# Kernel tuning notes

Measured on AMD Instinct MI355X. Metric: run time of the kernel, lower is better.

Reference implementation:

```python
import jax, jax.numpy as jnp
import numpy as np

T = 2048      # total tokens (single prefill sequence)
HID = 2048    # hidden_size
H = 16        # num k-heads == num v-heads
DK = 128      # key head dim
DV = 128      # value head dim
K = 4         # causal conv kernel width
EPS = 1e-6


def setup_inputs() -> dict:
    key = jax.random.key(0)
    ks = jax.random.split(key, 10)
    n = lambda k, shape, sc: (jax.random.normal(k, shape, jnp.float32) * sc)
    return {
        "hidden_states": n(ks[0], (T, HID), 1.0),
        "Wq": n(ks[1], (HID, H * DK), 0.02),
        "Wk": n(ks[2], (HID, H * DK), 0.02),
        "Wv": n(ks[3], (HID, H * DV), 0.02),
        "Wb": n(ks[4], (HID, H), 0.02),
        "conv_wq": n(ks[5], (H * DK, K), 0.5),
        "conv_wk": n(ks[6], (H * DK, K), 0.5),
        "conv_wv": n(ks[7], (H * DV, K), 0.5),
        "o_norm_w": jnp.ones((DV,), jnp.float32),
        "Wo": n(ks[8], (HID, HID), 0.02),
    }


def _causal_conv_silu(x, w):
    # x: [T, D], w: [D, K] depthwise causal conv, then SiLU (matches causal_conv1d_fn)
    xp = jnp.pad(x, ((K - 1, 0), (0, 0)))
    y = sum(xp[j:j + T] * w[:, j] for j in range(K))
    return jax.nn.silu(y)


def _l2norm(x):
    return x * jax.lax.rsqrt(jnp.sum(x * x, axis=-1, keepdims=True) + EPS)


def reference(hidden_states, Wq, Wk, Wv, Wb, conv_wq, conv_wk, conv_wv, o_norm_w, Wo):
    # projections [T, H*D]
    q = _causal_conv_silu(hidden_states @ Wq, conv_wq).reshape(T, H, DK)
    k = _causal_conv_silu(hidden_states @ Wk, conv_wk).reshape(T, H, DK)
    v = _causal_conv_silu(hidden_states @ Wv, conv_wv).reshape(T, H, DV)
    beta = jax.nn.sigmoid(hidden_states @ Wb)  # [T, H]

    # qk l2-norm + scale (FLA chunk_delta_rule defaults)
    q = _l2norm(q) * (DK ** -0.5)
    k = _l2norm(k)

    # delta-rule recurrence: S <- S + beta * k (v - k^T S)
    def step(S, inp):
        q_t, k_t, v_t, b_t = inp            # [H,DK],[H,DK],[H,DV],[H]
        kS = jnp.einsum('hk,hkv->hv', k_t, S)
        delta = b_t[:, None] * (v_t - kS)   # [H, DV]
        S = S + jnp.einsum('hk,hv->hkv', k_t, delta)
        o_t = jnp.einsum('hk,hkv->hv', q_t, S)
        return S, o_t

    S0 = jnp.zeros((H, DK, DV), jnp.float32)
    _, o = jax.lax.scan(step, S0, (q, k, v, beta))  # o: [T, H, DV]

    # per-head RMSNorm on value head dim
    o = o * jax.lax.rsqrt(jnp.mean(o * o, axis=-1, keepdims=True) + EPS) * o_norm_w
    out = o.reshape(T, H * DV) @ Wo
    return out
```

## Files before the change

kernel.cpp:

```cpp
#include <hip/hip_runtime.h>

typedef unsigned short u16;
typedef __attribute__((ext_vector_type(4))) unsigned short u16x4;
typedef __attribute__((ext_vector_type(8))) unsigned short u16x8;
typedef __attribute__((ext_vector_type(8))) short short8;
typedef __attribute__((ext_vector_type(4))) float f32x4;

#define DEVI __device__ __forceinline__

DEVI u16 f2b(float f) {
  union { float f; unsigned u; } x; x.f = f;
  unsigned r = (x.u + 0x7fffu + ((x.u >> 16) & 1u)) >> 16;
  return (u16)r;
}
DEVI float b2f(u16 h) {
  union { unsigned u; float f; } x; x.u = ((unsigned)h) << 16;
  return x.f;
}
DEVI f32x4 mfma_bf16(short8 a, short8 b, f32x4 c) {
  return __builtin_amdgcn_mfma_f32_16x16x32_bf16(a, b, c, 0, 0, 0);
}
DEVI void gl2lds16(const u16* g, u16* l) {
  __builtin_amdgcn_global_load_lds((__attribute__((address_space(1))) void*)g,
                                   (__attribute__((address_space(3))) void*)l,
                                   16, 0, 0);
}
DEVI void barrier_lds() {
  asm volatile("s_waitcnt lgkmcnt(0)\n\ts_barrier" ::: "memory");
}

__global__ void k_cvt(const float* __restrict__ src, u16* __restrict__ dst, int n4) {
  int i = blockIdx.x * 256 + threadIdx.x;
  if (i < n4) {
    float4 v = ((const float4*)src)[i];
    u16x4 r; r.x = f2b(v.x); r.y = f2b(v.y); r.z = f2b(v.z); r.w = f2b(v.w);
    ((u16x4*)dst)[i] = r;
  }
}

__global__ void k_transpose(const float* __restrict__ src, u16* __restrict__ dst, int R, int C) {
  __shared__ float tile[32][33];
  int bx = blockIdx.x << 5, by = blockIdx.y << 5;
  int x = threadIdx.x, y = threadIdx.y;
#pragma unroll
  for (int j = 0; j < 32; j += 8)
    tile[y + j][x] = src[(size_t)(by + y + j) * C + bx + x];
  __syncthreads();
#pragma unroll
  for (int j = 0; j < 32; j += 8)
    dst[(size_t)(bx + y + j) * R + by + x] = f2b(tile[x][y + j]);
}

__global__ __launch_bounds__(256, 2)
void k_gemm_bt(const u16* __restrict__ A, const u16* __restrict__ BT,
               float* __restrict__ Cf, u16* __restrict__ Cb,
               int M, int N, int K, int outbf) {
  __shared__ __align__(16) u16 As[4096];
  __shared__ __align__(16) u16 Bs[4096];
  const int tid = threadIdx.x, wave = tid >> 6, lane = tid & 63;
  const long bm = (long)blockIdx.y << 7, bn = (long)blockIdx.x << 7;
  const int r0 = (wave << 4) + (lane >> 2), kof = (lane & 3) << 3;
  const u16* gA = A + (bm + r0) * (long)K + kof;
  const u16* gB = BT + (bn + r0) * (long)K + kof;
  u16* lA = As + (wave << 9);
  u16* lB = Bs + (wave << 9);
  const long stepR = (long)64 * K;
  const int wr = (wave >> 1) << 6, wc = (wave & 1) << 6;
  const int fr = lane & 15, fq = (lane >> 4) << 3;
  f32x4 acc[4][4];
#pragma unroll
  for (int i = 0; i < 4; ++i)
#pragma unroll
    for (int j = 0; j < 4; ++j) acc[i][j] = (f32x4){0.f, 0.f, 0.f, 0.f};
  for (int k0 = 0; k0 < K; k0 += 32) {
    gl2lds16(gA + k0, lA);
    gl2lds16(gA + stepR + k0, lA + 2048);
    gl2lds16(gB + k0, lB);
    gl2lds16(gB + stepR + k0, lB + 2048);
    __syncthreads();
    short8 af[4], bfr[4];
#pragma unroll
    for (int t = 0; t < 4; ++t)
      af[t] = *(const short8*)&As[(wr + (t << 4) + fr) * 32 + fq];
#pragma unroll
    for (int t = 0; t < 4; ++t)
      bfr[t] = *(const short8*)&Bs[(wc + (t << 4) + fr) * 32 + fq];
#pragma unroll
    for (int i = 0; i < 4; ++i)
#pragma unroll
      for (int j = 0; j < 4; ++j)
        acc[i][j] = mfma_bf16(af[i], bfr[j], acc[i][j]);
    __syncthreads();
  }
  const int er = (lane >> 4) << 2, ec = lane & 15;
#pragma unroll
  for (int i = 0; i < 4; ++i)
#pragma unroll
    for (int j = 0; j < 4; ++j)
#pragma unroll
      for (int r = 0; r < 4; ++r) {
        long row = bm + wr + (i << 4) + er + r;
        long col = bn + wc + (j << 4) + ec;
        if (outbf) Cb[row * N + col] = f2b(acc[i][j][r]);
        else       Cf[row * N + col] = acc[i][j][r];
      }
}

__global__ void k_wbT(const float* __restrict__ src, u16* __restrict__ dst) {
  int j = blockIdx.x * 256 + threadIdx.x;
  int n = j >> 11, k = j & 2047;
  dst[j] = f2b(src[k * 16 + n]);
}

__global__ __launch_bounds__(256, 4)
void k_beta(const u16* __restrict__ Xb, const u16* __restrict__ WbT,
            float* __restrict__ beta) {
  __shared__ float part[4][256];
  int tid = threadIdx.x, w = tid >> 6, lane = tid & 63;
  int t0 = blockIdx.x << 4;
  int fr = lane & 15, fq = (lane >> 4) << 3;
  const u16* ap = Xb + (size_t)(t0 + fr) * 2048 + (w << 9) + fq;
  const u16* bp = WbT + (size_t)fr * 2048 + (w << 9) + fq;
  f32x4 acc = {0.f, 0.f, 0.f, 0.f};
#pragma unroll
  for (int ks = 0; ks < 16; ++ks)
    acc = mfma_bf16(*(const short8*)(ap + (ks << 5)), *(const short8*)(bp + (ks << 5)), acc);
  int er = (lane >> 4) << 2;
#pragma unroll
  for (int r = 0; r < 4; ++r) part[w][(er + r) * 16 + fr] = acc[r];
  __syncthreads();
  float s = part[0][tid] + part[1][tid] + part[2][tid] + part[3][tid];
  beta[(t0 << 4) + tid] = 1.f / (1.f + __expf(-s));
}

__global__ void k_conv(const u16* __restrict__ qkv,
                       const float* __restrict__ cwq, const float* __restrict__ cwk,
                       const float* __restrict__ cwv,
                       u16* __restrict__ qn, u16* __restrict__ kn, u16* __restrict__ vn) {
  int t = blockIdx.x, s = blockIdx.y;
  int kind = s >> 4, h = s & 15, d = threadIdx.x;
  int col = kind * 2048 + (h << 7) + d;
  const float* cw = (kind == 0) ? cwq : ((kind == 1) ? cwk : cwv);
  float4 w = *(const float4*)(cw + (size_t)((h << 7) + d) * 4);
  float x[4];
#pragma unroll
  for (int j = 0; j < 4; ++j) {
    int tt = t - 3 + j;
    x[j] = (tt >= 0) ? b2f(qkv[(size_t)tt * 6144 + col]) : 0.f;
  }
  float y = x[0] * w.x + x[1] * w.y + x[2] * w.z + x[3] * w.w;
  y = y / (1.f + __expf(-y));
  float sc = 1.f;
  __shared__ float red[2];
  if (kind < 2) {
    float ss = y * y;
#pragma unroll
    for (int off = 32; off; off >>= 1) ss += __shfl_down(ss, off, 64);
    int lane = threadIdx.x & 63, wv = threadIdx.x >> 6;
    if (lane == 0) red[wv] = ss;
    __syncthreads();
    float tot = red[0] + red[1];
    sc = rsqrtf(tot + 1e-6f);
    if (kind == 0) sc *= 0.08838834764831843f;
  }
  u16* dst = (kind == 0) ? qn : ((kind == 1) ? kn : vn);
  dst[((size_t)h << 18) + ((size_t)t << 7) + d] = f2b(y * sc);
}

__global__ __launch_bounds__(256, 2)
void k_prep(const u16* __restrict__ qn, const u16* __restrict__ kn, const u16* __restrict__ vn,
            const float* __restrict__ beta,
            u16* __restrict__ Gg, u16* __restrict__ Wg,
            u16* __restrict__ KTg, u16* __restrict__ UTg) {
  __shared__ __align__(16) char sm[70912];
  u16*  Kc  = (u16*)sm;
  u16*  Qc  = (u16*)(sm + 17408);
  u16*  Vc  = (u16*)(sm + 34816);
  u16*  KTl = (u16*)(sm + 52224);
  float* AL = (float*)(sm + 52224);
  float* Bl = (float*)(sm + 70656);
  u16*  WR  = Qc;
  int h = blockIdx.x, c = blockIdx.y;
  int tid = threadIdx.x, wave = tid >> 6, lane = tid & 63;
  size_t ch = (size_t)(c * 16 + h);
  const u16* kb = kn + ((size_t)h << 18) + ((size_t)c << 13);
  const u16* qb = qn + ((size_t)h << 18) + ((size_t)c << 13);
  const u16* vb = vn + ((size_t)h << 18) + ((size_t)c << 13);
#pragma unroll
  for (int s = 0; s < 4; ++s) {
    int e = (tid + (s << 8)) << 3;
    int t = e >> 7, d = e & 127;
    *(u16x8*)&Kc[t * 136 + d] = *(const u16x8*)(kb + e);
    *(u16x8*)&Qc[t * 136 + d] = *(const u16x8*)(qb + e);
    *(u16x8*)&Vc[t * 136 + d] = *(const u16x8*)(vb + e);
  }
  if (tid < 64) Bl[tid] = beta[((c << 6) + tid) * 16 + h];
  __syncthreads();
  int fr = lane & 15, fq = (lane >> 4) << 3, q4 = (lane >> 4) << 2;
  int arow = (wave << 4) + fr;
  f32x4 kk[4], qk[4];
#pragma unroll
  for (int ct = 0; ct < 4; ++ct) { kk[ct] = (f32x4){0.f,0.f,0.f,0.f}; qk[ct] = (f32x4){0.f,0.f,0.f,0.f}; }
#pragma unroll
  for (int ks = 0; ks < 4; ++ks) {
    short8 aK = *(const short8*)&Kc[arow * 136 + (ks << 5) + fq];
    short8 aQ = *(const short8*)&Qc[arow * 136 + (ks << 5) + fq];
#pragma unroll
    for (int ct = 0; ct < 4; ++ct) {
      short8 bK = *(const short8*)&Kc[((ct << 4) + fr) * 136 + (ks << 5) + fq];
      kk[ct] = mfma_bf16(aK, bK, kk[ct]);
      qk[ct] = mfma_bf16(aQ, bK, qk[ct]);
    }
  }
#pragma unroll
  for (int ct = 0; ct < 4; ++ct)
#pragma unroll
    for (int r = 0; r < 4; ++r) {
      int i = (wave << 4) + q4 + r, j = (ct << 4) + fr;
      Gg[(ch << 12) + i * 64 + j] = f2b((j <= i) ? qk[ct][r] : 0.f);
    }
  {
    int d = tid & 127, tg = tid >> 7;
#pragma unroll
    for (int it = 0; it < 4; ++it) {
      int t0 = (tg + (it << 1)) << 3;
      u16x8 pk;
#pragma unroll
      for (int j = 0; j < 8; ++j) pk[j] = Kc[(t0 + j) * 136 + d];
      *(u16x8*)&KTl[d * 72 + t0] = pk;
    }
  }
  __syncthreads();
#pragma unroll
  for (int it = 0; it < 4; ++it) {
    int idx = tid + (it << 8);
    int row = idx >> 3, j8 = (idx & 7) << 3;
    *(u16x8*)(KTg + (ch << 13) + (row << 6) + j8) = *(const u16x8*)&KTl[row * 72 + j8];
  }
  __syncthreads();
  {
    float bi[4];
#pragma unroll
    for (int r = 0; r < 4; ++r) bi[r] = Bl[(wave << 4) + q4 + r];
#pragma unroll
    for (int ct = 0; ct < 4; ++ct)
#pragma unroll
      for (int r = 0; r < 4; ++r) {
        int i = (wave << 4) + q4 + r, j = (ct << 4) + fr;
        AL[i * 64 + j] = (j < i) ? bi[r] * kk[ct][r] : 0.f;
      }
  }
  __syncthreads();
  float X[64];
  {
    const u16* colp = (tid < 128) ? (Kc + tid) : (Vc + (tid - 128));
#pragma unroll
    for (int t = 0; t < 64; ++t) X[t] = Bl[t] * b2f(colp[t * 136]);
#pragma unroll
    for (int r = 1; r < 64; ++r) {
      float s = 0.f;
      const float* Ar = &AL[r * 64];
      int r4 = r & ~3;
#pragma unroll
      for (int l = 0; l < 64; l += 4)
        if (l + 4 <= r) {
          float4 a = *(const float4*)(Ar + l);
          s += a.x * X[l] + a.y * X[l + 1] + a.z * X[l + 2] + a.w * X[l + 3];
        }
#pragma unroll
      for (int l = 0; l < 4; ++l)
        if (r4 + l < r) s += Ar[r4 + l] * X[r4 + l];
      X[r] -= s;
    }
  }
  __syncthreads();
  if (tid < 128) {
#pragma unroll
    for (int t = 0; t < 64; ++t) WR[t * 136 + tid] = f2b(X[t]);
  } else {
    int v = tid - 128;
    u16* dstr = UTg + (ch << 13) + (v << 6);
#pragma unroll
    for (int j = 0; j < 8; ++j) {
      u16x8 p;
#pragma unroll
      for (int e = 0; e < 8; ++e) p[e] = f2b(X[(j << 3) + e]);
      *(u16x8*)(dstr + (j << 3)) = p;
    }
  }
  __syncthreads();
#pragma unroll
  for (int it = 0; it < 4; ++it) {
    int idx = tid + (it << 8);
    int row = idx >> 4, j8 = (idx & 15) << 3;
    *(u16x8*)(Wg + (ch << 13) + (row << 7) + j8) = *(const u16x8*)&WR[row * 136 + j8];
  }
}

struct Frags { short8 q[4], w[4], g[2], k[4]; u16x4 u; };

DEVI void load_frags(Frags& f, const u16* qh, const u16* Wg, const u16* Gg,
                     const u16* KTg, const u16* UTg, int c, int h,
                     int trow, int fr, int fq, int q4, int w, int vbase) {
  const u16* qb = qh + ((size_t)((c << 6) + trow + fr) << 7) + fq;
#pragma unroll
  for (int ks = 0; ks < 4; ++ks) f.q[ks] = *(const short8*)(qb + (ks << 5));
  size_t ch = (size_t)(c * 16 + h);
  const u16* wb = Wg + (ch << 13) + ((size_t)(trow + fr) << 7) + fq;
#pragma unroll
  for (int ks = 0; ks < 4; ++ks) f.w[ks] = *(const short8*)(wb + (ks << 5));
  const u16* gb = Gg + (ch << 12) + ((size_t)(trow + fr) << 6) + fq;
#pragma unroll
  for (int ks = 0; ks < 2; ++ks) f.g[ks] = *(const short8*)(gb + (ks << 5));
  const u16* kbp = KTg + (ch << 13) + ((size_t)(w << 5) << 6) + fq;
#pragma unroll
  for (int dt = 0; dt < 2; ++dt)
#pragma unroll
    for (int ks = 0; ks < 2; ++ks)
      f.k[(dt << 1) | ks] = *(const short8*)(kbp + ((size_t)((dt << 4) + fr) << 6) + (ks << 5));
  f.u = *(const u16x4*)(UTg + (ch << 13) + ((size_t)(vbase + fr) << 6) + trow + q4);
}

DEVI void chunk_body(int c, Frags& f, u16* ST, u16* DT, float* oh,
                     int trow, int fr, int fq, int q4, int w, int vbase,
                     f32x4& S0, f32x4& S1) {
#pragma unroll
  for (int r = 0; r < 4; ++r) {
    ST[(q4 + r) * 136 + (w << 5) + fr] = f2b(S0[r]);
    ST[(q4 + r) * 136 + (w << 5) + 16 + fr] = f2b(S1[r]);
  }
  barrier_lds();
  short8 sf[4];
#pragma unroll
  for (int ks = 0; ks < 4; ++ks) sf[ks] = *(const short8*)&ST[fr * 136 + (ks << 5) + fq];
  f32x4 racc = {0.f,0.f,0.f,0.f}, oacc = {0.f,0.f,0.f,0.f};
#pragma unroll
  for (int ks = 0; ks < 4; ++ks) {
    racc = mfma_bf16(f.w[ks], sf[ks], racc);
    oacc = mfma_bf16(f.q[ks], sf[ks], oacc);
  }
#pragma unroll
  for (int r = 0; r < 4; ++r)
    DT[fr * 72 + trow + q4 + r] = f2b(b2f(f.u[r]) - racc[r]);
  barrier_lds();
  short8 df[2];
#pragma unroll
  for (int ks = 0; ks < 2; ++ks) df[ks] = *(const short8*)&DT[fr * 72 + (ks << 5) + fq];
#pragma unroll
  for (int ks = 0; ks < 2; ++ks) {
    oacc = mfma_bf16(f.g[ks], df[ks], oacc);
    S0 = mfma_bf16(df[ks], f.k[ks], S0);
    S1 = mfma_bf16(df[ks], f.k[2 | ks], S1);
  }
#pragma unroll
  for (int r = 0; r < 4; ++r)
    oh[(size_t)((c << 6) + trow + q4 + r) * 128 + vbase + fr] = oacc[r];
}

__global__ __launch_bounds__(256, 1)
void k_delta(const u16* __restrict__ qn, const u16* __restrict__ Wg,
             const u16* __restrict__ Gg, const u16* __restrict__ KTg,
             const u16* __restrict__ UTg, float* __restrict__ o) {
  __shared__ __align__(16) u16 ST[16 * 136];
  __shared__ __align__(16) u16 DT[16 * 72];
  int bx = blockIdx.x;
  int h = bx & 15, vbase = (bx >> 4) << 4;
  int tid = threadIdx.x, w = tid >> 6, lane = tid & 63;
  int fr = lane & 15, fq = (lane >> 4) << 3, q4 = (lane >> 4) << 2;
  int trow = w << 4;
  const u16* qh = qn + ((size_t)h << 18);
  float* oh = o + ((size_t)h << 18);
  f32x4 S0 = {0.f,0.f,0.f,0.f}, S1 = {0.f,0.f,0.f,0.f};
  Frags fa, fb;
  load_frags(fa, qh, Wg, Gg, KTg, UTg, 0, h, trow, fr, fq, q4, w, vbase);
  for (int c = 0; c < 32; c += 2) {
    int c1 = c + 1, c2 = (c + 2 < 32) ? c + 2 : 31;
    load_frags(fb, qh, Wg, Gg, KTg, UTg, c1, h, trow, fr, fq, q4, w, vbase);
    chunk_body(c, fa, ST, DT, oh, trow, fr, fq, q4, w, vbase, S0, S1);
    load_frags(fa, qh, Wg, Gg, KTg, UTg, c2, h, trow, fr, fq, q4, w, vbase);
    chunk_body(c1, fb, ST, DT, oh, trow, fr, fq, q4, w, vbase, S0, S1);
  }
}

__global__ void k_onorm(const float* __restrict__ o, const float* __restrict__ onw,
                        u16* __restrict__ onb) {
  int t = blockIdx.x, h = blockIdx.y, d = threadIdx.x;
  float x = o[((size_t)h << 18) + ((size_t)t << 7) + d];
  float ss = x * x;
#pragma unroll
  for (int off = 32; off; off >>= 1) ss += __shfl_down(ss, off, 64);
  __shared__ float red[2];
  int lane = d & 63, wv = d >> 6;
  if (lane == 0) red[wv] = ss;
  __syncthreads();
  float tot = red[0] + red[1];
  float y = x * rsqrtf(tot * (1.f / 128.f) + 1e-6f) * onw[d];
  onb[((size_t)t << 11) + (h << 7) + d] = f2b(y);
}

extern "C" void kernel_launch(void* const* d_in, const int* in_sizes, int n_in,
                              void* d_out, int out_size, void* d_ws, size_t ws_size,
                              hipStream_t stream) {
  (void)in_sizes; (void)n_in; (void)out_size; (void)ws_size;
  const float* hs  = (const float*)d_in[0];
  const float* Wq  = (const float*)d_in[1];
  const float* Wk  = (const float*)d_in[2];
  const float* Wv  = (const float*)d_in[3];
  const float* Wb  = (const float*)d_in[4];
  const float* cwq = (const float*)d_in[5];
  const float* cwk = (const float*)d_in[6];
  const float* cwv = (const float*)d_in[7];
  const float* onw = (const float*)d_in[8];
  const float* Wo  = (const float*)d_in[9];
  float* out = (float*)d_out;
  char* ws = (char*)d_ws;
  const size_t MB = 1ull << 20;
  u16*  Xb   = (u16*)(ws);
  u16*  WT   = (u16*)(ws + 8  * MB);
  u16*  WoT  = (u16*)(ws + 32 * MB);
  u16*  QKV  = (u16*)(ws + 40 * MB);
  u16*  Wg   = (u16*)(ws + 40 * MB);
  u16*  KTg  = (u16*)(ws + 48 * MB);
  u16*  UTg  = (u16*)(ws + 56 * MB);
  u16*  qn_  = (u16*)(ws + 64 * MB);
  u16*  kn_  = (u16*)(ws + 72 * MB);
  u16*  vn_  = (u16*)(ws + 80 * MB);
  float* beta= (float*)(ws + 88 * MB);
  u16*  WbT  = (u16*)(ws + 88 * MB + 512 * 1024);
  u16*  Gm   = (u16*)(ws + 89 * MB);
  float* o_  = (float*)(ws + 93 * MB);
  u16*  onb  = (u16*)(ws + 109 * MB);

  dim3 tb(32, 8);
  k_cvt<<<4096, 256, 0, stream>>>(hs, Xb, 2048 * 2048 / 4);
  k_wbT<<<128, 256, 0, stream>>>(Wb, WbT);
  k_transpose<<<dim3(64, 64), tb, 0, stream>>>(Wq, WT,                   2048, 2048);
  k_transpose<<<dim3(64, 64), tb, 0, stream>>>(Wk, WT + 2048 * 2048,     2048, 2048);
  k_transpose<<<dim3(64, 64), tb, 0, stream>>>(Wv, WT + 2 * 2048 * 2048, 2048, 2048);
  k_transpose<<<dim3(64, 64), tb, 0, stream>>>(Wo, WoT,                  2048, 2048);
  k_gemm_bt<<<dim3(48, 16), 256, 0, stream>>>(Xb, WT, nullptr, QKV, 2048, 6144, 2048, 1);
  k_beta<<<128, 256, 0, stream>>>(Xb, WbT, beta);
  k_conv<<<dim3(2048, 48), 128, 0, stream>>>(QKV, cwq, cwk, cwv, qn_, kn_, vn_);
  k_prep<<<dim3(16, 32), 256, 0, stream>>>(qn_, kn_, vn_, beta, Gm, Wg, KTg, UTg);
  k_delta<<<128, 256, 0, stream>>>(qn_, Wg, Gm, KTg, UTg, o_);
  k_onorm<<<dim3(2048, 16), 128, 0, stream>>>(o_, onw, onb);
  k_gemm_bt<<<dim3(16, 16), 256, 0, stream>>>(onb, WoT, out, nullptr, 2048, 2048, 2048, 0);
}
```

Baseline: 399.6 us.

## Fuse preprocessing launches, widen transpose tiles, and swizzle GEMM LDS layout

```diff
diff --git a/kernel.cpp b/kernel.cpp
--- a/kernel.cpp
+++ b/kernel.cpp
@@ -29,26 +29,45 @@
   asm volatile("s_waitcnt lgkmcnt(0)\n\ts_barrier" ::: "memory");
 }
 
-__global__ void k_cvt(const float* __restrict__ src, u16* __restrict__ dst, int n4) {
-  int i = blockIdx.x * 256 + threadIdx.x;
-  if (i < n4) {
-    float4 v = ((const float4*)src)[i];
-    u16x4 r; r.x = f2b(v.x); r.y = f2b(v.y); r.z = f2b(v.z); r.w = f2b(v.w);
-    ((u16x4*)dst)[i] = r;
-  }
-}
-
-__global__ void k_transpose(const float* __restrict__ src, u16* __restrict__ dst, int R, int C) {
-  __shared__ float tile[32][33];
-  int bx = blockIdx.x << 5, by = blockIdx.y << 5;
-  int x = threadIdx.x, y = threadIdx.y;
-#pragma unroll
-  for (int j = 0; j < 32; j += 8)
-    tile[y + j][x] = src[(size_t)(by + y + j) * C + bx + x];
-  __syncthreads();
-#pragma unroll
-  for (int j = 0; j < 32; j += 8)
-    dst[(size_t)(bx + y + j) * R + by + x] = f2b(tile[x][y + j]);
+__global__ void k_cvt(const float* __restrict__ src, u16* __restrict__ dst, int n4,
+                      const float* __restrict__ Wb, u16* __restrict__ WbT) {
+  int b = blockIdx.x;
+  if (b < 4096) {
+    int i = b * 256 + threadIdx.x;
+    if (i < n4) {
+      float4 v = ((const float4*)src)[i];
+      u16x4 r; r.x = f2b(v.x); r.y = f2b(v.y); r.z = f2b(v.z); r.w = f2b(v.w);
+      ((u16x4*)dst)[i] = r;
+    }
+  } else {
+    int j = (b - 4096) * 256 + threadIdx.x;
+    int n = j >> 11, k = j & 2047;
+    WbT[j] = f2b(Wb[k * 16 + n]);
+  }
+}
+
+__global__ __launch_bounds__(256)
+void k_transpose4(const float* __restrict__ s0, const float* __restrict__ s1,
+                  const float* __restrict__ s2, const float* __restrict__ s3,
+                  u16* __restrict__ d0, u16* __restrict__ d1,
+                  u16* __restrict__ d2, u16* __restrict__ d3) {
+  const int RC = 2048;
+  const float* src = (blockIdx.z == 0) ? s0 : (blockIdx.z == 1) ? s1 : (blockIdx.z == 2) ? s2 : s3;
+  u16* dst = (blockIdx.z == 0) ? d0 : (blockIdx.z == 1) ? d1 : (blockIdx.z == 2) ? d2 : d3;
+  __shared__ u16 tile[64 * 66];
+  int bx = blockIdx.x << 6, by = blockIdx.y << 6;
+  int x = threadIdx.x & 63, g = threadIdx.x >> 6;
+#pragma unroll
+  for (int i = 0; i < 16; ++i) {
+    int r = (i << 2) + g;
+    tile[x * 66 + r] = f2b(src[(size_t)(by + r) * RC + bx + x]);
+  }
+  __syncthreads();
+#pragma unroll
+  for (int i = 0; i < 16; ++i) {
+    int r = (i << 2) + g;
+    dst[(size_t)(bx + r) * RC + by + x] = tile[r * 66 + x];
+  }
 }
 
 __global__ __launch_bounds__(256, 2)
@@ -59,7 +78,8 @@
   __shared__ __align__(16) u16 Bs[4096];
   const int tid = threadIdx.x, wave = tid >> 6, lane = tid & 63;
   const long bm = (long)blockIdx.y << 7, bn = (long)blockIdx.x << 7;
-  const int r0 = (wave << 4) + (lane >> 2), kof = (lane & 3) << 3;
+  const int r0 = (wave << 4) + (lane >> 2);
+  const int kof = (((lane & 3) ^ ((lane >> 3) & 3)) << 3);
   const u16* gA = A + (bm + r0) * (long)K + kof;
   const u16* gB = BT + (bn + r0) * (long)K + kof;
   u16* lA = As + (wave << 9);
@@ -67,6 +87,8 @@
   const long stepR = (long)64 * K;
   const int wr = (wave >> 1) << 6, wc = (wave & 1) << 6;
   const int fr = lane & 15, fq = (lane >> 4) << 3;
+  const int sw = ((fr >> 1) & 3) << 3;
+  const int fqs = fq ^ sw;
   f32x4 acc[4][4];
 #pragma unroll
   for (int i = 0; i < 4; ++i)
@@ -81,10 +103,10 @@
     short8 af[4], bfr[4];
 #pragma unroll
     for (int t = 0; t < 4; ++t)
-      af[t] = *(const short8*)&As[(wr + (t << 4) + fr) * 32 + fq];
+      af[t] = *(const short8*)&As[(wr + (t << 4) + fr) * 32 + fqs];
 #pragma unroll
     for (int t = 0; t < 4; ++t)
-      bfr[t] = *(const short8*)&Bs[(wc + (t << 4) + fr) * 32 + fq];
+      bfr[t] = *(const short8*)&Bs[(wc + (t << 4) + fr) * 32 + fqs];
 #pragma unroll
     for (int i = 0; i < 4; ++i)
 #pragma unroll
@@ -104,12 +126,6 @@
         if (outbf) Cb[row * N + col] = f2b(acc[i][j][r]);
         else       Cf[row * N + col] = acc[i][j][r];
       }
-}
-
-__global__ void k_wbT(const float* __restrict__ src, u16* __restrict__ dst) {
-  int j = blockIdx.x * 256 + threadIdx.x;
-  int n = j >> 11, k = j & 2047;
-  dst[j] = f2b(src[k * 16 + n]);
 }
 
 __global__ __launch_bounds__(256, 4)
@@ -431,13 +447,9 @@
   float* o_  = (float*)(ws + 93 * MB);
   u16*  onb  = (u16*)(ws + 109 * MB);
 
-  dim3 tb(32, 8);
-  k_cvt<<<4096, 256, 0, stream>>>(hs, Xb, 2048 * 2048 / 4);
-  k_wbT<<<128, 256, 0, stream>>>(Wb, WbT);
-  k_transpose<<<dim3(64, 64), tb, 0, stream>>>(Wq, WT,                   2048, 2048);
-  k_transpose<<<dim3(64, 64), tb, 0, stream>>>(Wk, WT + 2048 * 2048,     2048, 2048);
-  k_transpose<<<dim3(64, 64), tb, 0, stream>>>(Wv, WT + 2 * 2048 * 2048, 2048, 2048);
-  k_transpose<<<dim3(64, 64), tb, 0, stream>>>(Wo, WoT,                  2048, 2048);
+  k_cvt<<<4224, 256, 0, stream>>>(hs, Xb, 2048 * 2048 / 4, Wb, WbT);
+  k_transpose4<<<dim3(32, 32, 4), 256, 0, stream>>>(
+      Wq, Wk, Wv, Wo, WT, WT + 2048 * 2048, WT + 2 * 2048 * 2048, WoT);
   k_gemm_bt<<<dim3(48, 16), 256, 0, stream>>>(Xb, WT, nullptr, QKV, 2048, 6144, 2048, 1);
   k_beta<<<128, 256, 0, stream>>>(Xb, WbT, beta);
   k_conv<<<dim3(2048, 48), 128, 0, stream>>>(QKV, cwq, cwk, cwv, qn_, kn_, vn_);
```

After: 388.8 us. 1.03x faster.
